# Kernel optimization log

Hardware: AMD Instinct MI355X
Metric: run time of the kernel (lower is better)

Reference implementation:

```python
import jax, jax.numpy as jnp
import numpy as np

N_NODES = 50000
N_EDGES = 400000
D_IN = 512
D_OUT = 512
MASK_RATE = 0.3


def setup_inputs() -> dict:
    key = jax.random.key(0)
    k1, k2, k3, k4, k5 = jax.random.split(key, 5)
    feat = jax.random.normal(k1, (N_NODES, D_IN), dtype=jnp.float32)
    # xavier_uniform for weight [in_feat, out_feat]
    limit = float(np.sqrt(6.0 / (D_IN + D_OUT)))
    weight = jax.random.uniform(k2, (D_IN, D_OUT), dtype=jnp.float32, minval=-limit, maxval=limit)
    edge_src = jax.random.randint(k3, (N_EDGES,), 0, N_NODES, dtype=jnp.int64 if jax.config.jax_enable_x64 else jnp.int32)
    edge_dst = jax.random.randint(k4, (N_EDGES,), 0, N_NODES, dtype=jnp.int64 if jax.config.jax_enable_x64 else jnp.int32)
    edge_val = jax.random.uniform(k5, (N_EDGES,), dtype=jnp.float32)
    # deterministic stand-in for torch.randperm(...)[:num_mask]
    perm = jax.random.permutation(jax.random.fold_in(key, 7), N_NODES)
    mask_idx = perm[: int(MASK_RATE * N_NODES)]
    return {
        "feat": feat,
        "weight": weight,
        "edge_val": edge_val,
        "edge_src": edge_src,
        "edge_dst": edge_dst,
        "mask_idx": mask_idx,
    }


def reference(feat, weight, edge_val, edge_src, edge_dst, mask_idx):
    # zero out masked node rows (encoding_mask_noise)
    out_x = feat.at[mask_idx].set(0.0)
    # dense transform: [N, D_in] @ [D_in, D_out]
    x = out_x @ weight
    # spmm(adj, x): for edge (src -> dst, val): out[dst] += val * x[src]
    msgs = edge_val[:, None] * x[edge_src]  # [E, D_out]
    out = jax.ops.segment_sum(msgs, edge_dst, num_segments=feat.shape[0])
    return out, mask_idx
```

## Files before the change

### kernel.cpp

```cpp
#include <hip/hip_runtime.h>

#define DD 512
#define SCAN_B 256
#define BM 128
#define BN 128
#define BK 32
#define NSTEP 16
typedef unsigned short u16;
typedef unsigned int u32;
typedef unsigned char u8;

typedef __attribute__((ext_vector_type(8))) __bf16 bf16v8;
typedef __attribute__((ext_vector_type(2))) __bf16 bf16v2;
typedef __attribute__((ext_vector_type(4))) float f32x4;

__device__ __forceinline__ u32 pk2(float a, float b) {
  bf16v2 v;
  v[0] = (__bf16)a;
  v[1] = (__bf16)b;
  return __builtin_bit_cast(u32, v);
}
__device__ __forceinline__ u16 f2bf(float f) {
  return __builtin_bit_cast(u16, (__bf16)f);
}
__device__ __forceinline__ float bf2f(u32 h) {
  return __builtin_bit_cast(float, h << 16);
}

typedef const __attribute__((address_space(1))) void* gptr_t;
typedef __attribute__((address_space(3))) void* lptr_t;
__device__ __forceinline__ void gload_lds16(const void* g, void* l) {
  __builtin_amdgcn_global_load_lds((gptr_t)g, (lptr_t)l, 16, 0, 0);
}

#define BAR_N(N)                                                        \
  do {                                                                  \
    __builtin_amdgcn_sched_barrier(0);                                  \
    asm volatile("s_waitcnt vmcnt(" #N ") lgkmcnt(0)\n\ts_barrier" ::: "memory"); \
  } while (0)

__global__ __launch_bounds__(256) void wconv_t(const float* __restrict__ W,
                                               u16* __restrict__ Wt) {
  __shared__ float sm[64][65];
  const int bx = blockIdx.x;
  const int by = blockIdx.y;
  const int t = threadIdx.x;
  const int r = t >> 6;
  const int c = t & 63;
#pragma unroll
  for (int i = 0; i < 64; i += 4)
    sm[i + r][c] = W[(size_t)(bx * 64 + i + r) * DD + by * 64 + c];
  __syncthreads();
#pragma unroll
  for (int i = 0; i < 64; i += 4) {
    const int n = by * 64 + i + r;
    const int k = bx * 64 + c;
    Wt[(size_t)n * DD + k] = f2bf(sm[c][i + r]);
  }
}

__global__ __launch_bounds__(512) void gemm_pipe(const float* __restrict__ A,
                                                 const u16* __restrict__ Bt,
                                                 u16* __restrict__ X,
                                                 const u8* __restrict__ flg, int M) {
  __shared__ __align__(16) u16 ldsA[2][BM * BK];
  __shared__ __align__(16) u16 ldsB[3][BN * BK];
  const int tid = threadIdx.x;
  const int lane = tid & 63;
  const int w = tid >> 6;
  const int wm = w >> 2;
  const int wn = w & 3;

  const int nwg = gridDim.x;
  const int b = blockIdx.x;
  const int xcd = b & 7, j = b >> 3;
  const int q = nwg >> 3, r_ = nwg & 7;
  const int unit = (xcd < r_ ? xcd * (q + 1) : r_ * (q + 1) + (xcd - r_) * q) + j;
  const int row0 = (unit >> 2) * BM;
  const int colB = (unit & 3) * BN;

  const int lr = lane & 15;
  const int kg = lane >> 4;

  f32x4 acc[4][2] = {};

  const int arow = tid >> 2;
  const int agk = (tid & 3) ^ ((arow >> 1) & 3);
  int ar = row0 + arow;
  if (ar >= M) ar = M - 1;
  const float* gA = A + (size_t)ar * DD + agk * 8;
  const int laoff = tid * 8;
  const u32 akeep = flg[ar] ? 0u : 0xFFFFFFFFu;

  const int bcol = tid >> 2;
  const int bgk = (tid & 3) ^ ((bcol >> 1) & 3);
  const u16* gB = Bt + (size_t)(colB + bcol) * DD + bgk * 8;
  const int lboff = tid * 8;

  f32x4 rP[2][2];

  gload_lds16(gB, &ldsB[0][lboff]);
  gload_lds16(gB + BK, &ldsB[1][lboff]);
  rP[0][0] = *(const f32x4*)(gA);
  rP[0][1] = *(const f32x4*)(gA + 4);
  rP[1][0] = *(const f32x4*)(gA + BK);
  rP[1][1] = *(const f32x4*)(gA + BK + 4);
  {
    uint4 pk;
    pk.x = pk2(rP[0][0].x, rP[0][0].y) & akeep;
    pk.y = pk2(rP[0][0].z, rP[0][0].w) & akeep;
    pk.z = pk2(rP[0][1].x, rP[0][1].y) & akeep;
    pk.w = pk2(rP[0][1].z, rP[0][1].w) & akeep;
    *(uint4*)&ldsA[0][laoff] = pk;
  }
  BAR_N(2);

#pragma unroll
  for (int t = 0; t < NSTEP; ++t) {
    if (t + 2 < NSTEP)
      gload_lds16(gB + (t + 2) * BK, &ldsB[(t + 2) % 3][lboff]);
    if (t + 2 < NSTEP) {
      rP[t & 1][0] = *(const f32x4*)(gA + (t + 2) * BK);
      rP[t & 1][1] = *(const f32x4*)(gA + (t + 2) * BK + 4);
    }
    __builtin_amdgcn_sched_barrier(0);

    bf16v8 af[4], bfr[2];
#pragma unroll
    for (int m = 0; m < 4; ++m) {
      const int row = wm * 64 + m * 16 + lr;
      const int kc = kg ^ ((row >> 1) & 3);
      af[m] = *(const bf16v8*)&ldsA[t & 1][row * BK + kc * 8];
    }
#pragma unroll
    for (int n = 0; n < 2; ++n) {
      const int col = wn * 32 + n * 16 + lr;
      const int kc = kg ^ ((col >> 1) & 3);
      bfr[n] = *(const bf16v8*)&ldsB[t % 3][col * BK + kc * 8];
    }
#pragma unroll
    for (int m = 0; m < 4; ++m)
#pragma unroll
      for (int n = 0; n < 2; ++n)
        acc[m][n] = __builtin_amdgcn_mfma_f32_16x16x32_bf16(af[m], bfr[n], acc[m][n], 0, 0, 0);

    if (t + 1 < NSTEP) {
      uint4 pk;
      pk.x = pk2(rP[(t + 1) & 1][0].x, rP[(t + 1) & 1][0].y) & akeep;
      pk.y = pk2(rP[(t + 1) & 1][0].z, rP[(t + 1) & 1][0].w) & akeep;
      pk.z = pk2(rP[(t + 1) & 1][1].x, rP[(t + 1) & 1][1].y) & akeep;
      pk.w = pk2(rP[(t + 1) & 1][1].z, rP[(t + 1) & 1][1].w) & akeep;
      *(uint4*)&ldsA[(t + 1) & 1][laoff] = pk;
    }

    if (t < NSTEP - 3)      BAR_N(3);
    else if (t < NSTEP - 1) BAR_N(0);
  }

  const int crow = (lane >> 4) * 4;
  const int ccol = lane & 15;
#pragma unroll
  for (int m = 0; m < 4; ++m) {
    const int rowb = row0 + wm * 64 + m * 16 + crow;
#pragma unroll
    for (int n = 0; n < 2; ++n) {
      const int col = colB + wn * 32 + n * 16 + ccol;
#pragma unroll
      for (int r = 0; r < 4; ++r)
        X[(size_t)(rowb + r) * DD + col] = f2bf(acc[m][n][r]);
    }
  }
}

__global__ __launch_bounds__(256) void flag_build(const int* __restrict__ mask,
                                                  u8* __restrict__ flg,
                                                  float* __restrict__ out_tail, int nm) {
  const int i = blockIdx.x * blockDim.x + threadIdx.x;
  if (i < nm) {
    const int r = mask[i];
    flg[r] = 1;
    out_tail[i] = (float)r;
  }
}

__global__ __launch_bounds__(256) void hist(const int* __restrict__ dst,
                                            int* __restrict__ counts, int n) {
  const int i = blockIdx.x * blockDim.x + threadIdx.x;
  if (i < n) atomicAdd(&counts[dst[i]], 1);
}

__global__ __launch_bounds__(SCAN_B) void scanA(const int* __restrict__ counts,
                                                int* __restrict__ lscan,
                                                int* __restrict__ blockSums, int n) {
  __shared__ int sm[SCAN_B];
  const int t = threadIdx.x;
  const int i = blockIdx.x * SCAN_B + t;
  const int v = (i < n) ? counts[i] : 0;
  sm[t] = v;
  __syncthreads();
  for (int off = 1; off < SCAN_B; off <<= 1) {
    int add = (t >= off) ? sm[t - off] : 0;
    __syncthreads();
    sm[t] += add;
    __syncthreads();
  }
  if (i < n) lscan[i] = sm[t] - v;
  if (t == SCAN_B - 1) blockSums[blockIdx.x] = sm[t];
}

__global__ __launch_bounds__(SCAN_B) void scanC(int* __restrict__ lscan,
                                                const int* __restrict__ blockSums,
                                                int* __restrict__ cursor, int n, int nb) {
  __shared__ int sm[SCAN_B];
  const int t = threadIdx.x;
  const int v = (t < nb) ? blockSums[t] : 0;
  sm[t] = v;
  __syncthreads();
  for (int off = 1; off < SCAN_B; off <<= 1) {
    int add = (t >= off) ? sm[t - off] : 0;
    __syncthreads();
    sm[t] += add;
    __syncthreads();
  }
  const int base = sm[blockIdx.x] - ((blockIdx.x < nb) ? blockSums[blockIdx.x] : 0);
  const int i = blockIdx.x * SCAN_B + t;
  if (i < n) {
    const int o = lscan[i] + base;
    lscan[i] = o;
    cursor[i] = o;
  }
}

__global__ __launch_bounds__(256) void scatter_sort(const int* __restrict__ src,
                                                    const int* __restrict__ dst,
                                                    const float* __restrict__ ev,
                                                    int* __restrict__ cursor,
                                                    int* __restrict__ ssrc,
                                                    float* __restrict__ sval, int n) {
  const int i = blockIdx.x * blockDim.x + threadIdx.x;
  if (i < n) {
    const int pos = atomicAdd(&cursor[dst[i]], 1);
    ssrc[pos] = src[i];
    sval[pos] = ev[i];
  }
}

__global__ __launch_bounds__(256) void aggregate(const u16* __restrict__ x,
                                                 const int* __restrict__ ssrc,
                                                 const float* __restrict__ sval,
                                                 const int* __restrict__ offsets,
                                                 const int* __restrict__ counts,
                                                 float* __restrict__ out, int n_nodes) {
  const int node = blockIdx.x * 4 + (threadIdx.x >> 6);
  if (node >= n_nodes) return;
  const int lane = threadIdx.x & 63;
  const int b = offsets[node];
  const int e = b + counts[node];
  float acc[8] = {};
  int j = b;
#define AGG1(U, V)                                      \
  do {                                                  \
    acc[0] = fmaf(V, bf2f(U.x & 0xffffu), acc[0]);      \
    acc[1] = fmaf(V, bf2f(U.x >> 16),     acc[1]);      \
    acc[2] = fmaf(V, bf2f(U.y & 0xffffu), acc[2]);      \
    acc[3] = fmaf(V, bf2f(U.y >> 16),     acc[3]);      \
    acc[4] = fmaf(V, bf2f(U.z & 0xffffu), acc[4]);      \
    acc[5] = fmaf(V, bf2f(U.z >> 16),     acc[5]);      \
    acc[6] = fmaf(V, bf2f(U.w & 0xffffu), acc[6]);      \
    acc[7] = fmaf(V, bf2f(U.w >> 16),     acc[7]);      \
  } while (0)
  for (; j + 4 <= e; j += 4) {
    const int s0 = ssrc[j], s1 = ssrc[j + 1], s2 = ssrc[j + 2], s3 = ssrc[j + 3];
    const float v0 = sval[j], v1 = sval[j + 1], v2 = sval[j + 2], v3 = sval[j + 3];
    const uint4 u0 = *(const uint4*)(x + (size_t)s0 * DD + lane * 8);
    const uint4 u1 = *(const uint4*)(x + (size_t)s1 * DD + lane * 8);
    const uint4 u2 = *(const uint4*)(x + (size_t)s2 * DD + lane * 8);
    const uint4 u3 = *(const uint4*)(x + (size_t)s3 * DD + lane * 8);
    AGG1(u0, v0); AGG1(u1, v1); AGG1(u2, v2); AGG1(u3, v3);
  }
  for (; j < e; ++j) {
    const int s = ssrc[j];
    const float v = sval[j];
    const uint4 u = *(const uint4*)(x + (size_t)s * DD + lane * 8);
    AGG1(u, v);
  }
#undef AGG1
  f32x4* o = (f32x4*)(out + (size_t)node * DD + lane * 8);
  f32x4 o0 = {acc[0], acc[1], acc[2], acc[3]};
  f32x4 o1 = {acc[4], acc[5], acc[6], acc[7]};
  __builtin_nontemporal_store(o0, o);
  __builtin_nontemporal_store(o1, o + 1);
}

extern "C" void kernel_launch(void* const* d_in, const int* in_sizes, int n_in,
                              void* d_out, int out_size, void* d_ws, size_t ws_size,
                              hipStream_t stream) {
  const float* feat     = (const float*)d_in[0];
  const float* weight   = (const float*)d_in[1];
  const float* edge_val = (const float*)d_in[2];
  const int*   edge_src = (const int*)d_in[3];
  const int*   edge_dst = (const int*)d_in[4];
  const int*   mask_idx = (const int*)d_in[5];

  const int n_nodes = in_sizes[0] / DD;
  const int n_edges = in_sizes[2];
  const int n_mask  = in_sizes[5];

  const int n_tiles_m = (n_nodes + BM - 1) / BM;
  const int m_pad = n_tiles_m * BM;

  float* out = (float*)d_out;

  char* base = (char*)d_ws;
  size_t off = 0;
  auto alloc = [&](size_t bytes) {
    void* p = base + off;
    off = (off + bytes + 255) & ~(size_t)255;
    return p;
  };
  u16*   x      = (u16*)alloc((size_t)m_pad * DD * sizeof(u16));
  u16*   wt     = (u16*)alloc((size_t)DD * DD * sizeof(u16));
  int*   counts = (int*)alloc((size_t)n_nodes * sizeof(int));
  u8*    flg    = (u8*)alloc((size_t)m_pad);
  const size_t zspan = (size_t)((char*)(flg + m_pad) - (char*)counts);
  int*   offs   = (int*)alloc((size_t)n_nodes * sizeof(int));
  int*   cursor = (int*)alloc((size_t)n_nodes * sizeof(int));
  int*   bsums  = (int*)alloc(SCAN_B * sizeof(int));
  int*   ssrc   = (int*)alloc((size_t)n_edges * sizeof(int));
  float* sval   = (float*)alloc((size_t)n_edges * sizeof(float));

  const int nb = (n_nodes + SCAN_B - 1) / SCAN_B;

  (void)hipMemsetAsync(counts, 0, zspan, stream);
  hist<<<(n_edges + 255) / 256, 256, 0, stream>>>(edge_dst, counts, n_edges);
  scanA<<<nb, SCAN_B, 0, stream>>>(counts, offs, bsums, n_nodes);
  scanC<<<nb, SCAN_B, 0, stream>>>(offs, bsums, cursor, n_nodes, nb);
  scatter_sort<<<(n_edges + 255) / 256, 256, 0, stream>>>(edge_src, edge_dst, edge_val,
                                                          cursor, ssrc, sval, n_edges);
  flag_build<<<(n_mask + 255) / 256, 256, 0, stream>>>(mask_idx, flg,
                                                       out + (size_t)n_nodes * DD, n_mask);

  dim3 wg(DD / 64, DD / 64);
  wconv_t<<<wg, 256, 0, stream>>>(weight, wt);
  const int nwg = (DD / BN) * n_tiles_m;
  gemm_pipe<<<nwg, 512, 0, stream>>>(feat, wt, x, flg, n_nodes);

  aggregate<<<(n_nodes + 3) / 4, 256, 0, stream>>>(x, ssrc, sval, offs, counts, out, n_nodes);
}
```

Measured before the change: 179.9 us.

## Double GEMM K-tile to 64 and pack sorted edge src/val pairs

Measured after the change: 178.1 us. No clear change (-1.0%).

```diff
diff --git a/kernel.cpp b/kernel.cpp
--- a/kernel.cpp
+++ b/kernel.cpp
@@ -4,8 +4,8 @@
 #define SCAN_B 256
 #define BM 128
 #define BN 128
-#define BK 32
-#define NSTEP 16
+#define BK 64
+#define NSTEP 8
 typedef unsigned short u16;
 typedef unsigned int u32;
 typedef unsigned char u8;
@@ -59,12 +59,12 @@
   }
 }
 
-__global__ __launch_bounds__(512) void gemm_pipe(const float* __restrict__ A,
-                                                 const u16* __restrict__ Bt,
-                                                 u16* __restrict__ X,
-                                                 const u8* __restrict__ flg, int M) {
+__global__ __launch_bounds__(512, 4) void gemm_pipe(const float* __restrict__ A,
+                                                    const u16* __restrict__ Bt,
+                                                    u16* __restrict__ X,
+                                                    const u8* __restrict__ flg, int M) {
   __shared__ __align__(16) u16 ldsA[2][BM * BK];
-  __shared__ __align__(16) u16 ldsB[3][BN * BK];
+  __shared__ __align__(16) u16 ldsB[2][BN * BK];
   const int tid = threadIdx.x;
   const int lane = tid & 63;
   const int w = tid >> 6;
@@ -73,9 +73,9 @@
 
   const int nwg = gridDim.x;
   const int b = blockIdx.x;
-  const int xcd = b & 7, j = b >> 3;
+  const int xcd = b & 7, jj = b >> 3;
   const int q = nwg >> 3, r_ = nwg & 7;
-  const int unit = (xcd < r_ ? xcd * (q + 1) : r_ * (q + 1) + (xcd - r_) * q) + j;
+  const int unit = (xcd < r_ ? xcd * (q + 1) : r_ * (q + 1) + (xcd - r_) * q) + jj;
   const int row0 = (unit >> 2) * BM;
   const int colB = (unit & 3) * BN;
 
@@ -84,76 +84,103 @@
 
   f32x4 acc[4][2] = {};
 
-  const int arow = tid >> 2;
-  const int agk = (tid & 3) ^ ((arow >> 1) & 3);
-  int ar = row0 + arow;
-  if (ar >= M) ar = M - 1;
-  const float* gA = A + (size_t)ar * DD + agk * 8;
-  const int laoff = tid * 8;
-  const u32 akeep = flg[ar] ? 0u : 0xFFFFFFFFu;
-
-  const int bcol = tid >> 2;
-  const int bgk = (tid & 3) ^ ((bcol >> 1) & 3);
-  const u16* gB = Bt + (size_t)(colB + bcol) * DD + bgk * 8;
-  const int lboff = tid * 8;
-
-  f32x4 rP[2][2];
-
-  gload_lds16(gB, &ldsB[0][lboff]);
-  gload_lds16(gB + BK, &ldsB[1][lboff]);
-  rP[0][0] = *(const f32x4*)(gA);
-  rP[0][1] = *(const f32x4*)(gA + 4);
-  rP[1][0] = *(const f32x4*)(gA + BK);
-  rP[1][1] = *(const f32x4*)(gA + BK + 4);
+  const int arow0 = tid >> 3;
+  const int as = tid & 7;
+  const int ag = as ^ (arow0 & 7);
+  int ar0 = row0 + arow0;      if (ar0 >= M) ar0 = M - 1;
+  int ar1 = row0 + arow0 + 64; if (ar1 >= M) ar1 = M - 1;
+  const float* gA0 = A + (size_t)ar0 * DD + ag * 8;
+  const float* gA1 = A + (size_t)ar1 * DD + ag * 8;
+  const int la0 = arow0 * BK + as * 8;
+  const int la1 = (arow0 + 64) * BK + as * 8;
+  const u32 akeep0 = flg[ar0] ? 0u : 0xFFFFFFFFu;
+  const u32 akeep1 = flg[ar1] ? 0u : 0xFFFFFFFFu;
+
+  const int bcol0 = tid >> 3, bs = tid & 7;
+  const int bg = bs ^ (bcol0 & 7);
+  const u16* gB0 = Bt + (size_t)(colB + bcol0) * DD + bg * 8;
+  const u16* gB1 = Bt + (size_t)(colB + bcol0 + 64) * DD + bg * 8;
+  const int lb0 = tid * 8, lb1 = (tid + 512) * 8;
+
+  f32x4 rP[3][4];
+
+  gload_lds16(gB0, &ldsB[0][lb0]);
+  gload_lds16(gB1, &ldsB[0][lb1]);
+#pragma unroll
+  for (int p = 0; p < 2; ++p) {
+    rP[p][0] = *(const f32x4*)(gA0 + p * BK);
+    rP[p][1] = *(const f32x4*)(gA0 + p * BK + 4);
+    rP[p][2] = *(const f32x4*)(gA1 + p * BK);
+    rP[p][3] = *(const f32x4*)(gA1 + p * BK + 4);
+  }
   {
-    uint4 pk;
-    pk.x = pk2(rP[0][0].x, rP[0][0].y) & akeep;
-    pk.y = pk2(rP[0][0].z, rP[0][0].w) & akeep;
-    pk.z = pk2(rP[0][1].x, rP[0][1].y) & akeep;
-    pk.w = pk2(rP[0][1].z, rP[0][1].w) & akeep;
-    *(uint4*)&ldsA[0][laoff] = pk;
-  }
-  BAR_N(2);
+    uint4 w0, w1;
+    w0.x = pk2(rP[0][0].x, rP[0][0].y) & akeep0;
+    w0.y = pk2(rP[0][0].z, rP[0][0].w) & akeep0;
+    w0.z = pk2(rP[0][1].x, rP[0][1].y) & akeep0;
+    w0.w = pk2(rP[0][1].z, rP[0][1].w) & akeep0;
+    w1.x = pk2(rP[0][2].x, rP[0][2].y) & akeep1;
+    w1.y = pk2(rP[0][2].z, rP[0][2].w) & akeep1;
+    w1.z = pk2(rP[0][3].x, rP[0][3].y) & akeep1;
+    w1.w = pk2(rP[0][3].z, rP[0][3].w) & akeep1;
+    *(uint4*)&ldsA[0][la0] = w0;
+    *(uint4*)&ldsA[0][la1] = w1;
+  }
+  BAR_N(4);
 
 #pragma unroll
   for (int t = 0; t < NSTEP; ++t) {
-    if (t + 2 < NSTEP)
-      gload_lds16(gB + (t + 2) * BK, &ldsB[(t + 2) % 3][lboff]);
+    if (t + 1 < NSTEP) {
+      gload_lds16(gB0 + (t + 1) * BK, &ldsB[(t + 1) & 1][lb0]);
+      gload_lds16(gB1 + (t + 1) * BK, &ldsB[(t + 1) & 1][lb1]);
+    }
     if (t + 2 < NSTEP) {
-      rP[t & 1][0] = *(const f32x4*)(gA + (t + 2) * BK);
-      rP[t & 1][1] = *(const f32x4*)(gA + (t + 2) * BK + 4);
-    }
-    __builtin_amdgcn_sched_barrier(0);
-
-    bf16v8 af[4], bfr[2];
-#pragma unroll
-    for (int m = 0; m < 4; ++m) {
-      const int row = wm * 64 + m * 16 + lr;
-      const int kc = kg ^ ((row >> 1) & 3);
-      af[m] = *(const bf16v8*)&ldsA[t & 1][row * BK + kc * 8];
-    }
-#pragma unroll
-    for (int n = 0; n < 2; ++n) {
-      const int col = wn * 32 + n * 16 + lr;
-      const int kc = kg ^ ((col >> 1) & 3);
-      bfr[n] = *(const bf16v8*)&ldsB[t % 3][col * BK + kc * 8];
-    }
-#pragma unroll
-    for (int m = 0; m < 4; ++m)
-#pragma unroll
-      for (int n = 0; n < 2; ++n)
-        acc[m][n] = __builtin_amdgcn_mfma_f32_16x16x32_bf16(af[m], bfr[n], acc[m][n], 0, 0, 0);
+      rP[(t + 2) % 3][0] = *(const f32x4*)(gA0 + (t + 2) * BK);
+      rP[(t + 2) % 3][1] = *(const f32x4*)(gA0 + (t + 2) * BK + 4);
+      rP[(t + 2) % 3][2] = *(const f32x4*)(gA1 + (t + 2) * BK);
+      rP[(t + 2) % 3][3] = *(const f32x4*)(gA1 + (t + 2) * BK + 4);
+    }
+
+#pragma unroll
+    for (int h = 0; h < 2; ++h) {
+      bf16v8 af[4], bfr[2];
+      const int c = h * 4 + kg;
+#pragma unroll
+      for (int m = 0; m < 4; ++m) {
+        const int row = wm * 64 + m * 16 + lr;
+        const int s = c ^ (row & 7);
+        af[m] = *(const bf16v8*)&ldsA[t & 1][row * BK + s * 8];
+      }
+#pragma unroll
+      for (int n = 0; n < 2; ++n) {
+        const int col = wn * 32 + n * 16 + lr;
+        const int s = c ^ (col & 7);
+        bfr[n] = *(const bf16v8*)&ldsB[t & 1][col * BK + s * 8];
+      }
+#pragma unroll
+      for (int m = 0; m < 4; ++m)
+#pragma unroll
+        for (int n = 0; n < 2; ++n)
+          acc[m][n] = __builtin_amdgcn_mfma_f32_16x16x32_bf16(af[m], bfr[n], acc[m][n], 0, 0, 0);
+    }
 
     if (t + 1 < NSTEP) {
-      uint4 pk;
-      pk.x = pk2(rP[(t + 1) & 1][0].x, rP[(t + 1) & 1][0].y) & akeep;
-      pk.y = pk2(rP[(t + 1) & 1][0].z, rP[(t + 1) & 1][0].w) & akeep;
-      pk.z = pk2(rP[(t + 1) & 1][1].x, rP[(t + 1) & 1][1].y) & akeep;
-      pk.w = pk2(rP[(t + 1) & 1][1].z, rP[(t + 1) & 1][1].w) & akeep;
-      *(uint4*)&ldsA[(t + 1) & 1][laoff] = pk;
-    }
-
-    if (t < NSTEP - 3)      BAR_N(3);
+      const f32x4 p0 = rP[(t + 1) % 3][0], p1 = rP[(t + 1) % 3][1];
+      const f32x4 p2 = rP[(t + 1) % 3][2], p3 = rP[(t + 1) % 3][3];
+      uint4 w0, w1;
+      w0.x = pk2(p0.x, p0.y) & akeep0;
+      w0.y = pk2(p0.z, p0.w) & akeep0;
+      w0.z = pk2(p1.x, p1.y) & akeep0;
+      w0.w = pk2(p1.z, p1.w) & akeep0;
+      w1.x = pk2(p2.x, p2.y) & akeep1;
+      w1.y = pk2(p2.z, p2.w) & akeep1;
+      w1.z = pk2(p3.x, p3.y) & akeep1;
+      w1.w = pk2(p3.z, p3.w) & akeep1;
+      *(uint4*)&ldsA[(t + 1) & 1][la0] = w0;
+      *(uint4*)&ldsA[(t + 1) & 1][la1] = w1;
+    }
+
+    if (t < NSTEP - 2)      BAR_N(4);
     else if (t < NSTEP - 1) BAR_N(0);
   }
 
@@ -235,19 +262,16 @@
                                                     const int* __restrict__ dst,
                                                     const float* __restrict__ ev,
                                                     int* __restrict__ cursor,
-                                                    int* __restrict__ ssrc,
-                                                    float* __restrict__ sval, int n) {
+                                                    int2* __restrict__ esp, int n) {
   const int i = blockIdx.x * blockDim.x + threadIdx.x;
   if (i < n) {
     const int pos = atomicAdd(&cursor[dst[i]], 1);
-    ssrc[pos] = src[i];
-    sval[pos] = ev[i];
+    esp[pos] = make_int2(src[i], __float_as_int(ev[i]));
   }
 }
 
 __global__ __launch_bounds__(256) void aggregate(const u16* __restrict__ x,
-                                                 const int* __restrict__ ssrc,
-                                                 const float* __restrict__ sval,
+                                                 const int2* __restrict__ esp,
                                                  const int* __restrict__ offsets,
                                                  const int* __restrict__ counts,
                                                  float* __restrict__ out, int n_nodes) {
@@ -270,19 +294,20 @@
     acc[7] = fmaf(V, bf2f(U.w >> 16),     acc[7]);      \
   } while (0)
   for (; j + 4 <= e; j += 4) {
-    const int s0 = ssrc[j], s1 = ssrc[j + 1], s2 = ssrc[j + 2], s3 = ssrc[j + 3];
-    const float v0 = sval[j], v1 = sval[j + 1], v2 = sval[j + 2], v3 = sval[j + 3];
-    const uint4 u0 = *(const uint4*)(x + (size_t)s0 * DD + lane * 8);
-    const uint4 u1 = *(const uint4*)(x + (size_t)s1 * DD + lane * 8);
-    const uint4 u2 = *(const uint4*)(x + (size_t)s2 * DD + lane * 8);
-    const uint4 u3 = *(const uint4*)(x + (size_t)s3 * DD + lane * 8);
-    AGG1(u0, v0); AGG1(u1, v1); AGG1(u2, v2); AGG1(u3, v3);
+    const int2 p0 = esp[j], p1 = esp[j + 1], p2 = esp[j + 2], p3 = esp[j + 3];
+    const uint4 u0 = *(const uint4*)(x + (size_t)p0.x * DD + lane * 8);
+    const uint4 u1 = *(const uint4*)(x + (size_t)p1.x * DD + lane * 8);
+    const uint4 u2 = *(const uint4*)(x + (size_t)p2.x * DD + lane * 8);
+    const uint4 u3 = *(const uint4*)(x + (size_t)p3.x * DD + lane * 8);
+    AGG1(u0, __int_as_float(p0.y));
+    AGG1(u1, __int_as_float(p1.y));
+    AGG1(u2, __int_as_float(p2.y));
+    AGG1(u3, __int_as_float(p3.y));
   }
   for (; j < e; ++j) {
-    const int s = ssrc[j];
-    const float v = sval[j];
-    const uint4 u = *(const uint4*)(x + (size_t)s * DD + lane * 8);
-    AGG1(u, v);
+    const int2 p = esp[j];
+    const uint4 u = *(const uint4*)(x + (size_t)p.x * DD + lane * 8);
+    AGG1(u, __int_as_float(p.y));
   }
 #undef AGG1
   f32x4* o = (f32x4*)(out + (size_t)node * DD + lane * 8);
@@ -326,8 +351,7 @@
   int*   offs   = (int*)alloc((size_t)n_nodes * sizeof(int));
   int*   cursor = (int*)alloc((size_t)n_nodes * sizeof(int));
   int*   bsums  = (int*)alloc(SCAN_B * sizeof(int));
-  int*   ssrc   = (int*)alloc((size_t)n_edges * sizeof(int));
-  float* sval   = (float*)alloc((size_t)n_edges * sizeof(float));
+  int2*  esp    = (int2*)alloc((size_t)n_edges * sizeof(int2));
 
   const int nb = (n_nodes + SCAN_B - 1) / SCAN_B;
 
@@ -336,7 +360,7 @@
   scanA<<<nb, SCAN_B, 0, stream>>>(counts, offs, bsums, n_nodes);
   scanC<<<nb, SCAN_B, 0, stream>>>(offs, bsums, cursor, n_nodes, nb);
   scatter_sort<<<(n_edges + 255) / 256, 256, 0, stream>>>(edge_src, edge_dst, edge_val,
-                                                          cursor, ssrc, sval, n_edges);
+                                                          cursor, esp, n_edges);
   flag_build<<<(n_mask + 255) / 256, 256, 0, stream>>>(mask_idx, flg,
                                                        out + (size_t)n_nodes * DD, n_mask);
 
@@ -345,5 +369,5 @@
   const int nwg = (DD / BN) * n_tiles_m;
   gemm_pipe<<<nwg, 512, 0, stream>>>(feat, wt, x, flg, n_nodes);
 
-  aggregate<<<(n_nodes + 3) / 4, 256, 0, stream>>>(x, ssrc, sval, offs, counts, out, n_nodes);
-}
+  aggregate<<<(n_nodes + 3) / 4, 256, 0, stream>>>(x, esp, offs, counts, out, n_nodes);
+}
```
